# Kernel optimization log

Measured on AMD Instinct MI355X. Metric: run time of the kernel, lower is better.

Reference implementation:

```python
import jax, jax.numpy as jnp
import numpy as np

N = 100000   # nodes
E = 1600000  # edges
G = 64       # graphs in batch
IN, H, F1, OUT = 3, 64, 256, 10
EPS = 1e-5


def setup_inputs() -> dict:
    key = jax.random.key(0)
    ks = jax.random.split(key, 16)
    d = {}
    d["x"] = jax.random.normal(ks[0], (N, IN), dtype=jnp.float32)
    d["membership"] = jnp.sort(jax.random.randint(ks[1], (N,), 0, G))
    d["edges"] = jax.random.randint(ks[2], (2, E), 0, N)
    def lin(k, fan_in, shape):
        return jax.random.uniform(k, shape, jnp.float32, -1.0, 1.0) / np.sqrt(fan_in)
    # GraphConv1: out = lin_rel(agg) + lin_root(x); lin_root has no bias in PyG
    d["W_rel1"] = lin(ks[3], IN, (IN, H)); d["b_rel1"] = jnp.zeros((H,), jnp.float32)
    d["W_root1"] = lin(ks[4], IN, (IN, H))
    d["W_rel2"] = lin(ks[5], H, (H, H)); d["b_rel2"] = jnp.zeros((H,), jnp.float32)
    d["W_root2"] = lin(ks[6], H, (H, H))
    d["g1"] = jnp.ones((H,), jnp.float32); d["b1"] = jnp.zeros((H,), jnp.float32)
    d["g2"] = jnp.ones((H,), jnp.float32); d["b2"] = jnp.zeros((H,), jnp.float32)
    d["W_fc1"] = lin(ks[7], H, (H, F1)); d["b_fc1"] = lin(ks[8], H, (F1,))
    d["g3"] = jnp.ones((F1,), jnp.float32); d["b3"] = jnp.zeros((F1,), jnp.float32)
    d["W_fc2"] = lin(ks[9], F1, (F1, OUT)); d["b_fc2"] = lin(ks[10], F1, (OUT,))
    return d


def _bn(h, g, b):
    # BatchNorm1d in training mode: biased batch variance
    m = h.mean(axis=0)
    v = h.var(axis=0)
    return (h - m) * jax.lax.rsqrt(v + EPS) * g + b


def reference(x, membership, edges, W_rel1, b_rel1, W_root1, W_rel2, b_rel2,
              W_root2, g1, b1, g2, b2, W_fc1, b_fc1, g3, b3, W_fc2, b_fc2):
    src, dst = edges[0], edges[1]

    def gconv(h, Wr, br, Wroot):
        # message = x_j (edge_weight=None); aggr='add' at target node
        agg = jax.ops.segment_sum(h[src], dst, num_segments=N)
        return agg @ Wr + br + h @ Wroot

    h = _bn(jax.nn.relu(gconv(x, W_rel1, b_rel1, W_root1)), g1, b1)
    h = _bn(jax.nn.relu(gconv(h, W_rel2, b_rel2, W_root2)), g2, b2)
    # global mean pool over graph membership
    cnt = jax.ops.segment_sum(jnp.ones((N,), h.dtype), membership, num_segments=G)
    pooled = jax.ops.segment_sum(h, membership, num_segments=G) / jnp.maximum(cnt, 1.0)[:, None]
    z = _bn(jax.nn.relu(pooled @ W_fc1 + b_fc1), g3, b3)
    return z @ W_fc2 + b_fc2
```

## Files before the change

### kernel.cpp

```cpp
#include <hip/hip_runtime.h>
#include <hip/hip_bf16.h>

#define EPSV 1e-5f
#define BKT 128
#define NB  782

typedef __hip_bfloat16 bf16;
typedef __attribute__((ext_vector_type(8))) short short8v;
typedef __attribute__((ext_vector_type(4))) float f32x4v;

__device__ inline void atomAddG(float* p, float v) { unsafeAtomicAdd(p, v); }
__device__ inline unsigned short f2bf(float v) {
    bf16 h = __float2bfloat16(v);
    return *reinterpret_cast<unsigned short*>(&h);
}

__global__ __launch_bounds__(256) void bhist_kernel(
    const int* __restrict__ edges, int* __restrict__ gbcnt, int E)
{
    __shared__ int lh[NB];
    const int t = threadIdx.x;
    for (int i = t; i < NB; i += 256) lh[i] = 0;
    __syncthreads();
    const int base = blockIdx.x * 4096;
    #pragma unroll
    for (int i = 0; i < 16; ++i) {
        int e = base + i * 256 + t;
        if (e < E) atomicAdd(&lh[edges[E + e] >> 7], 1);
    }
    __syncthreads();
    for (int i = t; i < NB; i += 256) {
        int c = lh[i];
        if (c) atomicAdd(&gbcnt[i], c);
    }
}

__global__ __launch_bounds__(256) void bscan_kernel(
    const int* __restrict__ gbcnt, int* __restrict__ bbase,
    int* __restrict__ gcursor, int E)
{
    __shared__ int l[256];
    const int t = threadIdx.x;
    int b0 = t * 4;
    int v0 = (b0 + 0 < NB) ? gbcnt[b0 + 0] : 0;
    int v1 = (b0 + 1 < NB) ? gbcnt[b0 + 1] : 0;
    int v2 = (b0 + 2 < NB) ? gbcnt[b0 + 2] : 0;
    int v3 = (b0 + 3 < NB) ? gbcnt[b0 + 3] : 0;
    int tot = v0 + v1 + v2 + v3;
    l[t] = tot;
    __syncthreads();
    for (int o = 1; o < 256; o <<= 1) {
        int add = (t >= o) ? l[t - o] : 0;
        __syncthreads();
        l[t] += add;
        __syncthreads();
    }
    int off = l[t] - tot;
    if (b0 + 0 < NB) { bbase[b0 + 0] = off;                gcursor[b0 + 0] = off; }
    if (b0 + 1 < NB) { bbase[b0 + 1] = off + v0;           gcursor[b0 + 1] = off + v0; }
    if (b0 + 2 < NB) { bbase[b0 + 2] = off + v0 + v1;      gcursor[b0 + 2] = off + v0 + v1; }
    if (b0 + 3 < NB) { bbase[b0 + 3] = off + v0 + v1 + v2; gcursor[b0 + 3] = off + v0 + v1 + v2; }
    if (t == 0) bbase[NB] = E;
}

__global__ __launch_bounds__(256) void bfill_kernel(
    const int* __restrict__ edges, int* __restrict__ gcursor,
    int* __restrict__ pk, int E)
{
    __shared__ int lh[NB];
    __shared__ int lbase[NB];
    const int t = threadIdx.x;
    for (int i = t; i < NB; i += 256) lh[i] = 0;
    __syncthreads();
    const int base = blockIdx.x * 4096;
    int dv[16];
    #pragma unroll
    for (int i = 0; i < 16; ++i) {
        int e = base + i * 256 + t;
        dv[i] = (e < E) ? edges[E + e] : -1;
        if (dv[i] >= 0) atomicAdd(&lh[dv[i] >> 7], 1);
    }
    __syncthreads();
    for (int i = t; i < NB; i += 256) {
        int c = lh[i];
        lbase[i] = c ? atomicAdd(&gcursor[i], c) : 0;
        lh[i] = 0;
    }
    __syncthreads();
    #pragma unroll
    for (int i = 0; i < 16; ++i) {
        int e = base + i * 256 + t;
        if (dv[i] >= 0) {
            int s = edges[e];
            int b = dv[i] >> 7;
            int pos = lbase[b] + atomicAdd(&lh[b], 1);
            pk[pos] = (s << 7) | (dv[i] & 127);
        }
    }
}

__global__ __launch_bounds__(256) void bsort_kernel(
    const int* __restrict__ pk, const int* __restrict__ bbase,
    const float* __restrict__ x,
    int* __restrict__ rowstart, int* __restrict__ srcs,
    float* __restrict__ agg1, int N, int E)
{
    __shared__ int lcnt[BKT];
    __shared__ int lscan[BKT];
    __shared__ float accx[BKT * 4];
    const int t = threadIdx.x;
    const int b = blockIdx.x;
    const int e0 = bbase[b], e1 = bbase[b + 1];
    if (t < BKT) lcnt[t] = 0;
    for (int i = t; i < BKT * 4; i += 256) accx[i] = 0.f;
    __syncthreads();
    for (int e = e0 + t; e < e1; e += 256) atomicAdd(&lcnt[pk[e] & 127], 1);
    __syncthreads();
    if (t < BKT) lscan[t] = lcnt[t];
    __syncthreads();
    for (int o = 1; o < BKT; o <<= 1) {
        int add = (t < BKT && t >= o) ? lscan[t - o] : 0;
        __syncthreads();
        if (t < BKT) lscan[t] += add;
        __syncthreads();
    }
    const int n0 = b * BKT;
    if (t < BKT) {
        int excl = lscan[t] - lcnt[t];
        lscan[t] = excl;
        int n = n0 + t;
        if (n <= N) rowstart[n] = e0 + excl;
        lcnt[t] = 0;
    }
    __syncthreads();
    for (int e = e0 + t; e < e1; e += 256) {
        int v = pk[e];
        int ld = v & 127;
        int s = v >> 7;
        int pos = atomicAdd(&lcnt[ld], 1);
        srcs[e0 + lscan[ld] + pos] = s;
        atomicAdd(&accx[ld * 4 + 0], x[s * 3 + 0]);
        atomicAdd(&accx[ld * 4 + 1], x[s * 3 + 1]);
        atomicAdd(&accx[ld * 4 + 2], x[s * 3 + 2]);
    }
    __syncthreads();
    for (int i = t; i < BKT * 3; i += 256) {
        int nl = i / 3, c = i - nl * 3;
        int n = n0 + nl;
        if (n < N) agg1[n * 3 + c] = accx[nl * 4 + c];
    }
}

__global__ __launch_bounds__(256) void bounds_kernel(
    const int* __restrict__ membership, int* __restrict__ gstart, int N)
{
    int n = blockIdx.x * 256 + threadIdx.x;
    if (n > N) return;
    int mp = (n == 0) ? -1 : membership[n - 1];
    int mc = (n == N) ? 64 : membership[n];
    for (int g = mp + 1; g <= mc; ++g) gstart[g] = n;
}

__global__ __launch_bounds__(256) void layer1_kernel(
    const float* __restrict__ x, const float* __restrict__ agg1,
    const float* __restrict__ W_rel1, const float* __restrict__ b_rel1,
    const float* __restrict__ W_root1,
    unsigned short* __restrict__ u1b, float* __restrict__ sums, float* __restrict__ sumsq,
    int N)
{
    const int t = threadIdx.x;
    const int f = t & 63, r4 = t >> 6;
    const float wr0 = W_rel1[f], wr1 = W_rel1[64 + f], wr2 = W_rel1[128 + f];
    const float wo0 = W_root1[f], wo1 = W_root1[64 + f], wo2 = W_root1[128 + f];
    const float bb = b_rel1[f];
    float ps = 0.f, pq = 0.f;
    const int base = blockIdx.x * 128;
    for (int i = r4; i < 128; i += 4) {
        int n = base + i;
        if (n >= N) break;
        float a0 = agg1[n * 3 + 0], a1 = agg1[n * 3 + 1], a2 = agg1[n * 3 + 2];
        float x0 = x[n * 3 + 0], x1 = x[n * 3 + 1], x2 = x[n * 3 + 2];
        float v = bb;
        v = fmaf(a0, wr0, v); v = fmaf(a1, wr1, v); v = fmaf(a2, wr2, v);
        v = fmaf(x0, wo0, v); v = fmaf(x1, wo1, v); v = fmaf(x2, wo2, v);
        v = fmaxf(v, 0.f);
        u1b[n * 64 + f] = f2bf(v);
        ps += v; pq += v * v;
    }
    __shared__ float lsum[4][64], lsq[4][64];
    lsum[r4][f] = ps; lsq[r4][f] = pq;
    __syncthreads();
    if (r4 == 0) {
        float s = lsum[0][f] + lsum[1][f] + lsum[2][f] + lsum[3][f];
        float q = lsq[0][f] + lsq[1][f] + lsq[2][f] + lsq[3][f];
        atomAddG(&sums[f], s);
        atomAddG(&sumsq[f], q);
    }
}

__global__ void bnscale_kernel(const float* __restrict__ sums, const float* __restrict__ sumsq,
                               const float* __restrict__ g, const float* __restrict__ b,
                               float invn, int C,
                               float* __restrict__ scale, float* __restrict__ shift)
{
    int f = blockIdx.x * blockDim.x + threadIdx.x;
    if (f >= C) return;
    float m = sums[f] * invn;
    float v = sumsq[f] * invn - m * m;
    float sc = g[f] * rsqrtf(v + EPSV);
    scale[f] = sc;
    shift[f] = b[f] - m * sc;
}

__global__ __launch_bounds__(256) void bnfold_kernel(
    const float* __restrict__ scale1, const float* __restrict__ shift1,
    const float* __restrict__ W_rel2, const float* __restrict__ W_root2,
    const float* __restrict__ b_rel2,
    unsigned short* __restrict__ wrelp, unsigned short* __restrict__ wrootp,
    float* __restrict__ crel, float* __restrict__ croot)
{
    __shared__ float r1[4][64], r2[4][64];
    const int t = threadIdx.x, f = t & 63, kg = t >> 6;
    float c1 = 0.f, c2 = 0.f;
    for (int k = kg * 16; k < kg * 16 + 16; ++k) {
        float sc = scale1[k], sh = shift1[k];
        float w1 = W_rel2[k * 64 + f], w2 = W_root2[k * 64 + f];
        wrelp[k * 64 + f] = f2bf(sc * w1);
        wrootp[k * 64 + f] = f2bf(sc * w2);
        c1 = fmaf(sh, w1, c1); c2 = fmaf(sh, w2, c2);
    }
    r1[kg][f] = c1; r2[kg][f] = c2;
    __syncthreads();
    if (kg == 0) {
        crel[f]  = r1[0][f] + r1[1][f] + r1[2][f] + r1[3][f];
        croot[f] = r2[0][f] + r2[1][f] + r2[2][f] + r2[3][f] + b_rel2[f];
    }
}

__global__ __launch_bounds__(256) void mfma_transform_kernel(
    const unsigned short* __restrict__ u1b,
    const unsigned short* __restrict__ wrelp, const unsigned short* __restrict__ wrootp,
    const float* __restrict__ crel, const float* __restrict__ croot,
    unsigned short* __restrict__ tb, unsigned short* __restrict__ pb, int NT)
{
    const int wid = (blockIdx.x * blockDim.x + threadIdx.x) >> 6;
    const int lane = threadIdx.x & 63;
    const int q = lane >> 4, r = lane & 15;

    short8v Bf[2][8];
    float cadd[8];
    #pragma unroll
    for (int kc = 0; kc < 2; ++kc) {
        #pragma unroll
        for (int ft = 0; ft < 8; ++ft) {
            const unsigned short* W = (ft < 4) ? wrelp : wrootp;
            const int f0 = (ft & 3) * 16;
            short8v b;
            #pragma unroll
            for (int j = 0; j < 8; ++j) {
                int k = 32 * kc + 8 * q + j;
                b[j] = (short)W[k * 64 + f0 + r];
            }
            Bf[kc][ft] = b;
        }
    }
    #pragma unroll
    for (int ft = 0; ft < 8; ++ft)
        cadd[ft] = (ft < 4) ? crel[(ft & 3) * 16 + r] : croot[(ft & 3) * 16 + r];

    const int totalWaves = (gridDim.x * blockDim.x) >> 6;
    for (int tile = wid; tile < NT; tile += totalWaves) {
        const int n0 = tile * 16;
        short8v A0 = *(const short8v*)&u1b[(n0 + r) * 64 + 8 * q];
        short8v A1 = *(const short8v*)&u1b[(n0 + r) * 64 + 32 + 8 * q];
        #pragma unroll
        for (int ft = 0; ft < 8; ++ft) {
            f32x4v d = {0.f, 0.f, 0.f, 0.f};
            d = __builtin_amdgcn_mfma_f32_16x16x32_bf16(A0, Bf[0][ft], d, 0, 0, 0);
            d = __builtin_amdgcn_mfma_f32_16x16x32_bf16(A1, Bf[1][ft], d, 0, 0, 0);
            unsigned short* O = (ft < 4) ? tb : pb;
            const int f0 = (ft & 3) * 16;
            const float ca = cadd[ft];
            #pragma unroll
            for (int rr = 0; rr < 4; ++rr) {
                int n = n0 + 4 * q + rr;
                O[n * 64 + f0 + r] = f2bf(d[rr] + ca);
            }
        }
    }
}

__global__ __launch_bounds__(256, 8) void gatherpool_kernel(
    const bf16* __restrict__ tb, const bf16* __restrict__ pb,
    const int* __restrict__ rowstart, const int* __restrict__ srcs,
    const int* __restrict__ membership,
    float* __restrict__ pooled, float* __restrict__ sums, float* __restrict__ sumsq,
    int N, int chunk)
{
    __shared__ float red[4][64];
    const int tid = threadIdx.x;
    const int w = tid >> 6, f = tid & 63;
    const int gw = __builtin_amdgcn_readfirstlane(blockIdx.x * 4 + w);
    const int n0 = gw * chunk;
    const int n1 = min(N, n0 + chunk);
    float ps = 0.f, pq = 0.f, pacc = 0.f;
    int curg = (n0 < N) ? membership[n0] : -1;

    for (int n = n0; n < n1; ++n) {
        int s0 = rowstart[n], s1 = rowstart[n + 1];
        float acc = __bfloat162float(pb[n * 64 + f]);
        int j = s0;
        for (; j + 15 < s1; j += 16) {
            float vs[16];
            #pragma unroll
            for (int q = 0; q < 16; ++q)
                vs[q] = __bfloat162float(tb[srcs[j + q] * 64 + f]);
            float sA = ((vs[0] + vs[1]) + (vs[2] + vs[3])) + ((vs[4] + vs[5]) + (vs[6] + vs[7]));
            float sB = ((vs[8] + vs[9]) + (vs[10] + vs[11])) + ((vs[12] + vs[13]) + (vs[14] + vs[15]));
            acc += sA + sB;
        }
        for (; j + 3 < s1; j += 4) {
            float v0 = __bfloat162float(tb[srcs[j + 0] * 64 + f]);
            float v1 = __bfloat162float(tb[srcs[j + 1] * 64 + f]);
            float v2 = __bfloat162float(tb[srcs[j + 2] * 64 + f]);
            float v3 = __bfloat162float(tb[srcs[j + 3] * 64 + f]);
            acc += (v0 + v1) + (v2 + v3);
        }
        for (; j < s1; ++j) acc += __bfloat162float(tb[srcs[j] * 64 + f]);

        acc = fmaxf(acc, 0.f);
        ps += acc; pq += acc * acc;

        int g = membership[n];
        if (g != curg) {
            atomAddG(&pooled[curg * 64 + f], pacc);
            pacc = 0.f;
            curg = g;
        }
        pacc += acc;
    }
    if (curg >= 0) atomAddG(&pooled[curg * 64 + f], pacc);

    red[w][f] = ps;
    __syncthreads();
    if (w == 0) atomAddG(&sums[f], red[0][f] + red[1][f] + red[2][f] + red[3][f]);
    __syncthreads();
    red[w][f] = pq;
    __syncthreads();
    if (w == 0) atomAddG(&sumsq[f], red[0][f] + red[1][f] + red[2][f] + red[3][f]);
}

__global__ __launch_bounds__(1024) void fc1_kernel(
    const float* __restrict__ pooled, const int* __restrict__ gstart,
    const float* __restrict__ scale2, const float* __restrict__ shift2,
    const float* __restrict__ W_fc1, const float* __restrict__ b_fc1,
    const float* __restrict__ g3, const float* __restrict__ b3,
    float* __restrict__ z)
{
    __shared__ float pm[4096];
    __shared__ float reds[4][256], redq[4][256];
    __shared__ float lsc[256], lsh[256];
    const int t = threadIdx.x;
    for (int i = t; i < 4096; i += 1024) {
        int g = i >> 6, f = i & 63;
        float c = fmaxf((float)(gstart[g + 1] - gstart[g]), 1.0f);
        pm[i] = fmaf(pooled[i] / c, scale2[f], shift2[f]);
    }
    __syncthreads();
    const int col = t & 255, grp = t >> 8;
    float acc[16];
    const float bc = b_fc1[col];
    #pragma unroll
    for (int g = 0; g < 16; ++g) acc[g] = bc;
    for (int k = 0; k < 64; ++k) {
        float wv = W_fc1[k * 256 + col];
        #pragma unroll
        for (int g = 0; g < 16; ++g)
            acc[g] = fmaf(pm[(grp * 16 + g) * 64 + k], wv, acc[g]);
    }
    float s = 0.f, q = 0.f;
    #pragma unroll
    for (int g = 0; g < 16; ++g) {
        acc[g] = fmaxf(acc[g], 0.f);
        s += acc[g]; q += acc[g] * acc[g];
    }
    reds[grp][col] = s; redq[grp][col] = q;
    __syncthreads();
    if (grp == 0) {
        float S = reds[0][col] + reds[1][col] + reds[2][col] + reds[3][col];
        float Q = redq[0][col] + redq[1][col] + redq[2][col] + redq[3][col];
        float m = S * (1.0f / 64.0f);
        float v = Q * (1.0f / 64.0f) - m * m;
        float sc = g3[col] * rsqrtf(v + EPSV);
        lsc[col] = sc;
        lsh[col] = b3[col] - m * sc;
    }
    __syncthreads();
    float sc = lsc[col], sh = lsh[col];
    #pragma unroll
    for (int g = 0; g < 16; ++g)
        z[(grp * 16 + g) * 256 + col] = fmaf(acc[g], sc, sh);
}

__global__ __launch_bounds__(640) void fc2_kernel(
    const float* __restrict__ z, const float* __restrict__ W_fc2,
    const float* __restrict__ b_fc2, float* __restrict__ out)
{
    int t = threadIdx.x;
    int g = t / 10, o = t % 10;
    float acc = b_fc2[o];
    for (int c = 0; c < 256; ++c)
        acc = fmaf(z[g * 256 + c], W_fc2[c * 10 + o], acc);
    out[g * 10 + o] = acc;
}

extern "C" void kernel_launch(void* const* d_in, const int* in_sizes, int n_in,
                              void* d_out, int out_size, void* d_ws, size_t ws_size,
                              hipStream_t stream) {
    const int N = 100000, E = 1600000;

    const float* x          = (const float*)d_in[0];
    const int*   membership = (const int*)d_in[1];
    const int*   edges      = (const int*)d_in[2];
    const float* W_rel1     = (const float*)d_in[3];
    const float* b_rel1     = (const float*)d_in[4];
    const float* W_root1    = (const float*)d_in[5];
    const float* W_rel2     = (const float*)d_in[6];
    const float* b_rel2     = (const float*)d_in[7];
    const float* W_root2    = (const float*)d_in[8];
    const float* g1         = (const float*)d_in[9];
    const float* b1         = (const float*)d_in[10];
    const float* g2         = (const float*)d_in[11];
    const float* b2         = (const float*)d_in[12];
    const float* W_fc1      = (const float*)d_in[13];
    const float* b_fc1      = (const float*)d_in[14];
    const float* g3         = (const float*)d_in[15];
    const float* b3         = (const float*)d_in[16];
    const float* W_fc2      = (const float*)d_in[17];
    const float* b_fc2      = (const float*)d_in[18];

    int*   wsi      = (int*)d_ws;
    float* wsf      = (float*)d_ws;
    int*   gbcnt    = wsi + 0;
    float* stats    = wsf + 784;
    float* pooled   = wsf + 1296;
    int*   bbase    = wsi + 5392;
    int*   gcursor  = wsi + 6192;
    int*   gstart   = wsi + 6976;
    int*   rowstart = wsi + 7104;
    int*   pk       = wsi + 107168;
    int*   srcs     = wsi + 1707168;
    float* agg1     = wsf + 3307168;
    unsigned short* u1b = (unsigned short*)(wsf + 3607200);
    unsigned short* tb  = (unsigned short*)(wsf + 6807200);
    unsigned short* pb  = (unsigned short*)(wsf + 10007200);
    unsigned short* wrelp  = (unsigned short*)(wsf + 13207200);
    unsigned short* wrootp = (unsigned short*)(wsf + 13209248);
    float* crel     = wsf + 13211296;
    float* croot    = wsf + 13211360;
    float* z        = wsf + 13211424;

    float* sums1  = stats + 0;
    float* sumsq1 = stats + 64;
    float* sums2  = stats + 128;
    float* sumsq2 = stats + 192;
    float* scale1 = stats + 256;
    float* shift1 = stats + 320;
    float* scale2 = stats + 384;
    float* shift2 = stats + 448;

    hipMemsetAsync(d_ws, 0, (size_t)(784 + 512 + 4096) * 4, stream);

    const int EB = (E + 4095) / 4096;
    bhist_kernel<<<EB, 256, 0, stream>>>(edges, gbcnt, E);
    bscan_kernel<<<1, 256, 0, stream>>>(gbcnt, bbase, gcursor, E);
    bfill_kernel<<<EB, 256, 0, stream>>>(edges, gcursor, pk, E);
    bsort_kernel<<<NB, 256, 0, stream>>>(pk, bbase, x, rowstart, srcs, agg1, N, E);
    bounds_kernel<<<(N + 256) / 256, 256, 0, stream>>>(membership, gstart, N);

    layer1_kernel<<<(N + 127) / 128, 256, 0, stream>>>(
        x, agg1, W_rel1, b_rel1, W_root1, u1b, sums1, sumsq1, N);
    bnscale_kernel<<<1, 64, 0, stream>>>(sums1, sumsq1, g1, b1, 1.0f / N, 64, scale1, shift1);

    bnfold_kernel<<<1, 256, 0, stream>>>(scale1, shift1, W_rel2, W_root2, b_rel2,
                                         wrelp, wrootp, crel, croot);
    mfma_transform_kernel<<<512, 256, 0, stream>>>(
        u1b, wrelp, wrootp, crel, croot, tb, pb, N / 16);

    {
        const int GRID2 = 2048;
        int chunk = (N + GRID2 * 4 - 1) / (GRID2 * 4);
        gatherpool_kernel<<<GRID2, 256, 0, stream>>>(
            (const bf16*)tb, (const bf16*)pb, rowstart, srcs, membership,
            pooled, sums2, sumsq2, N, chunk);
    }
    bnscale_kernel<<<1, 64, 0, stream>>>(sums2, sumsq2, g2, b2, 1.0f / N, 64, scale2, shift2);

    fc1_kernel<<<1, 1024, 0, stream>>>(pooled, gstart, scale2, shift2,
                                       W_fc1, b_fc1, g3, b3, z);
    fc2_kernel<<<1, 640, 0, stream>>>(z, W_fc2, b_fc2, (float*)d_out);
}
```

Baseline: 254.3 us.

## Vectorize edge gather to 4 edges per wave and fuse small kernels

The gather kernel now processes four edges in parallel per wave. Each 16-lane quarter loads 8-byte chunks (4 bf16 features) of a source row, and the partial sums are reduced with cross-lane shuffles. This replaces one 2-byte load per lane per edge and is meant to raise memory-level parallelism and use bytes per request better. Separately, the BN1 scale computation is folded into bnfold and fc2 is merged into fc1, removing two tiny kernel launches. The cost is shuffle reductions per node, and three quarters of the lanes sit idle during the per-node epilogue.

After: 265.0 us. 1.04x slower.

```diff
diff --git a/kernel.cpp b/kernel.cpp
--- a/kernel.cpp
+++ b/kernel.cpp
@@ -213,17 +213,27 @@
 }
 
 __global__ __launch_bounds__(256) void bnfold_kernel(
-    const float* __restrict__ scale1, const float* __restrict__ shift1,
+    const float* __restrict__ sums1, const float* __restrict__ sumsq1,
+    const float* __restrict__ g1, const float* __restrict__ b1,
     const float* __restrict__ W_rel2, const float* __restrict__ W_root2,
     const float* __restrict__ b_rel2,
     unsigned short* __restrict__ wrelp, unsigned short* __restrict__ wrootp,
-    float* __restrict__ crel, float* __restrict__ croot)
-{
+    float* __restrict__ crel, float* __restrict__ croot, float invn)
+{
+    __shared__ float lsc[64], lsh[64];
     __shared__ float r1[4][64], r2[4][64];
     const int t = threadIdx.x, f = t & 63, kg = t >> 6;
+    if (t < 64) {
+        float m = sums1[t] * invn;
+        float v = sumsq1[t] * invn - m * m;
+        float sc = g1[t] * rsqrtf(v + EPSV);
+        lsc[t] = sc;
+        lsh[t] = b1[t] - m * sc;
+    }
+    __syncthreads();
     float c1 = 0.f, c2 = 0.f;
     for (int k = kg * 16; k < kg * 16 + 16; ++k) {
-        float sc = scale1[k], sh = shift1[k];
+        float sc = lsc[k], sh = lsh[k];
         float w1 = W_rel2[k * 64 + f], w2 = W_root2[k * 64 + f];
         wrelp[k * 64 + f] = f2bf(sc * w1);
         wrootp[k * 64 + f] = f2bf(sc * w2);
@@ -255,13 +265,13 @@
         for (int ft = 0; ft < 8; ++ft) {
             const unsigned short* W = (ft < 4) ? wrelp : wrootp;
             const int f0 = (ft & 3) * 16;
-            short8v b;
+            short8v bb;
             #pragma unroll
             for (int j = 0; j < 8; ++j) {
                 int k = 32 * kc + 8 * q + j;
-                b[j] = (short)W[k * 64 + f0 + r];
+                bb[j] = (short)W[k * 64 + f0 + r];
             }
-            Bf[kc][ft] = b;
+            Bf[kc][ft] = bb;
         }
     }
     #pragma unroll
@@ -291,7 +301,7 @@
 }
 
 __global__ __launch_bounds__(256, 8) void gatherpool_kernel(
-    const bf16* __restrict__ tb, const bf16* __restrict__ pb,
+    const unsigned short* __restrict__ tb, const unsigned short* __restrict__ pb,
     const int* __restrict__ rowstart, const int* __restrict__ srcs,
     const int* __restrict__ membership,
     float* __restrict__ pooled, float* __restrict__ sums, float* __restrict__ sumsq,
@@ -299,63 +309,110 @@
 {
     __shared__ float red[4][64];
     const int tid = threadIdx.x;
-    const int w = tid >> 6, f = tid & 63;
-    const int gw = __builtin_amdgcn_readfirstlane(blockIdx.x * 4 + w);
+    const int w = tid >> 6, lane = tid & 63;
+    const int q = lane >> 4;
+    const int r = lane & 15;
+    const int gw = blockIdx.x * 4 + w;
     const int n0 = gw * chunk;
     const int n1 = min(N, n0 + chunk);
-    float ps = 0.f, pq = 0.f, pacc = 0.f;
+    float ps0 = 0.f, ps1 = 0.f, ps2 = 0.f, ps3 = 0.f;
+    float pq0 = 0.f, pq1 = 0.f, pq2 = 0.f, pq3 = 0.f;
+    float pa0 = 0.f, pa1 = 0.f, pa2 = 0.f, pa3 = 0.f;
     int curg = (n0 < N) ? membership[n0] : -1;
 
     for (int n = n0; n < n1; ++n) {
         int s0 = rowstart[n], s1 = rowstart[n + 1];
-        float acc = __bfloat162float(pb[n * 64 + f]);
+        float a0 = 0.f, a1 = 0.f, a2 = 0.f, a3 = 0.f;
         int j = s0;
-        for (; j + 15 < s1; j += 16) {
-            float vs[16];
+        for (; j + 31 < s1; j += 32) {
+            int idx[8];
+            uint2 v[8];
             #pragma unroll
-            for (int q = 0; q < 16; ++q)
-                vs[q] = __bfloat162float(tb[srcs[j + q] * 64 + f]);
-            float sA = ((vs[0] + vs[1]) + (vs[2] + vs[3])) + ((vs[4] + vs[5]) + (vs[6] + vs[7]));
-            float sB = ((vs[8] + vs[9]) + (vs[10] + vs[11])) + ((vs[12] + vs[13]) + (vs[14] + vs[15]));
-            acc += sA + sB;
+            for (int u = 0; u < 8; ++u) idx[u] = srcs[j + u * 4 + q];
+            #pragma unroll
+            for (int u = 0; u < 8; ++u)
+                v[u] = *(const uint2*)&tb[idx[u] * 64 + r * 4];
+            #pragma unroll
+            for (int u = 0; u < 8; ++u) {
+                a0 += __uint_as_float(v[u].x << 16);
+                a1 += __uint_as_float(v[u].x & 0xffff0000u);
+                a2 += __uint_as_float(v[u].y << 16);
+                a3 += __uint_as_float(v[u].y & 0xffff0000u);
+            }
         }
         for (; j + 3 < s1; j += 4) {
-            float v0 = __bfloat162float(tb[srcs[j + 0] * 64 + f]);
-            float v1 = __bfloat162float(tb[srcs[j + 1] * 64 + f]);
-            float v2 = __bfloat162float(tb[srcs[j + 2] * 64 + f]);
-            float v3 = __bfloat162float(tb[srcs[j + 3] * 64 + f]);
-            acc += (v0 + v1) + (v2 + v3);
-        }
-        for (; j < s1; ++j) acc += __bfloat162float(tb[srcs[j] * 64 + f]);
-
-        acc = fmaxf(acc, 0.f);
-        ps += acc; pq += acc * acc;
-
-        int g = membership[n];
-        if (g != curg) {
-            atomAddG(&pooled[curg * 64 + f], pacc);
-            pacc = 0.f;
-            curg = g;
-        }
-        pacc += acc;
-    }
-    if (curg >= 0) atomAddG(&pooled[curg * 64 + f], pacc);
-
-    red[w][f] = ps;
-    __syncthreads();
-    if (w == 0) atomAddG(&sums[f], red[0][f] + red[1][f] + red[2][f] + red[3][f]);
-    __syncthreads();
-    red[w][f] = pq;
-    __syncthreads();
-    if (w == 0) atomAddG(&sumsq[f], red[0][f] + red[1][f] + red[2][f] + red[3][f]);
-}
-
-__global__ __launch_bounds__(1024) void fc1_kernel(
+            int src = srcs[j + q];
+            uint2 vv = *(const uint2*)&tb[src * 64 + r * 4];
+            a0 += __uint_as_float(vv.x << 16);
+            a1 += __uint_as_float(vv.x & 0xffff0000u);
+            a2 += __uint_as_float(vv.y << 16);
+            a3 += __uint_as_float(vv.y & 0xffff0000u);
+        }
+        int rem = s1 - j;
+        if (q < rem) {
+            int src = srcs[j + q];
+            uint2 vv = *(const uint2*)&tb[src * 64 + r * 4];
+            a0 += __uint_as_float(vv.x << 16);
+            a1 += __uint_as_float(vv.x & 0xffff0000u);
+            a2 += __uint_as_float(vv.y << 16);
+            a3 += __uint_as_float(vv.y & 0xffff0000u);
+        }
+        a0 += __shfl_xor(a0, 16); a0 += __shfl_xor(a0, 32);
+        a1 += __shfl_xor(a1, 16); a1 += __shfl_xor(a1, 32);
+        a2 += __shfl_xor(a2, 16); a2 += __shfl_xor(a2, 32);
+        a3 += __shfl_xor(a3, 16); a3 += __shfl_xor(a3, 32);
+
+        if (q == 0) {
+            uint2 pv = *(const uint2*)&pb[n * 64 + r * 4];
+            a0 = fmaxf(a0 + __uint_as_float(pv.x << 16), 0.f);
+            a1 = fmaxf(a1 + __uint_as_float(pv.x & 0xffff0000u), 0.f);
+            a2 = fmaxf(a2 + __uint_as_float(pv.y << 16), 0.f);
+            a3 = fmaxf(a3 + __uint_as_float(pv.y & 0xffff0000u), 0.f);
+            ps0 += a0; pq0 += a0 * a0;
+            ps1 += a1; pq1 += a1 * a1;
+            ps2 += a2; pq2 += a2 * a2;
+            ps3 += a3; pq3 += a3 * a3;
+            int g = membership[n];
+            if (g != curg) {
+                atomAddG(&pooled[curg * 64 + 4 * r + 0], pa0);
+                atomAddG(&pooled[curg * 64 + 4 * r + 1], pa1);
+                atomAddG(&pooled[curg * 64 + 4 * r + 2], pa2);
+                atomAddG(&pooled[curg * 64 + 4 * r + 3], pa3);
+                pa0 = pa1 = pa2 = pa3 = 0.f;
+                curg = g;
+            }
+            pa0 += a0; pa1 += a1; pa2 += a2; pa3 += a3;
+        }
+    }
+    if (q == 0 && curg >= 0) {
+        atomAddG(&pooled[curg * 64 + 4 * r + 0], pa0);
+        atomAddG(&pooled[curg * 64 + 4 * r + 1], pa1);
+        atomAddG(&pooled[curg * 64 + 4 * r + 2], pa2);
+        atomAddG(&pooled[curg * 64 + 4 * r + 3], pa3);
+    }
+
+    if (q == 0) {
+        red[w][4 * r + 0] = ps0; red[w][4 * r + 1] = ps1;
+        red[w][4 * r + 2] = ps2; red[w][4 * r + 3] = ps3;
+    }
+    __syncthreads();
+    if (w == 0) atomAddG(&sums[lane], red[0][lane] + red[1][lane] + red[2][lane] + red[3][lane]);
+    __syncthreads();
+    if (q == 0) {
+        red[w][4 * r + 0] = pq0; red[w][4 * r + 1] = pq1;
+        red[w][4 * r + 2] = pq2; red[w][4 * r + 3] = pq3;
+    }
+    __syncthreads();
+    if (w == 0) atomAddG(&sumsq[lane], red[0][lane] + red[1][lane] + red[2][lane] + red[3][lane]);
+}
+
+__global__ __launch_bounds__(1024) void fc12_kernel(
     const float* __restrict__ pooled, const int* __restrict__ gstart,
     const float* __restrict__ scale2, const float* __restrict__ shift2,
     const float* __restrict__ W_fc1, const float* __restrict__ b_fc1,
     const float* __restrict__ g3, const float* __restrict__ b3,
-    float* __restrict__ z)
+    const float* __restrict__ W_fc2, const float* __restrict__ b_fc2,
+    float* __restrict__ z, float* __restrict__ out)
 {
     __shared__ float pm[4096];
     __shared__ float reds[4][256], redq[4][256];
@@ -400,18 +457,14 @@
     #pragma unroll
     for (int g = 0; g < 16; ++g)
         z[(grp * 16 + g) * 256 + col] = fmaf(acc[g], sc, sh);
-}
-
-__global__ __launch_bounds__(640) void fc2_kernel(
-    const float* __restrict__ z, const float* __restrict__ W_fc2,
-    const float* __restrict__ b_fc2, float* __restrict__ out)
-{
-    int t = threadIdx.x;
-    int g = t / 10, o = t % 10;
-    float acc = b_fc2[o];
-    for (int c = 0; c < 256; ++c)
-        acc = fmaf(z[g * 256 + c], W_fc2[c * 10 + o], acc);
-    out[g * 10 + o] = acc;
+    __syncthreads();
+    if (t < 640) {
+        int g = t / 10, o = t % 10;
+        float a = b_fc2[o];
+        for (int c = 0; c < 256; ++c)
+            a = fmaf(z[g * 256 + c], W_fc2[c * 10 + o], a);
+        out[g * 10 + o] = a;
+    }
 }
 
 extern "C" void kernel_launch(void* const* d_in, const int* in_sizes, int n_in,
@@ -464,8 +517,6 @@
     float* sumsq1 = stats + 64;
     float* sums2  = stats + 128;
     float* sumsq2 = stats + 192;
-    float* scale1 = stats + 256;
-    float* shift1 = stats + 320;
     float* scale2 = stats + 384;
     float* shift2 = stats + 448;
 
@@ -480,10 +531,10 @@
 
     layer1_kernel<<<(N + 127) / 128, 256, 0, stream>>>(
         x, agg1, W_rel1, b_rel1, W_root1, u1b, sums1, sumsq1, N);
-    bnscale_kernel<<<1, 64, 0, stream>>>(sums1, sumsq1, g1, b1, 1.0f / N, 64, scale1, shift1);
-
-    bnfold_kernel<<<1, 256, 0, stream>>>(scale1, shift1, W_rel2, W_root2, b_rel2,
-                                         wrelp, wrootp, crel, croot);
+
+    bnfold_kernel<<<1, 256, 0, stream>>>(sums1, sumsq1, g1, b1,
+                                         W_rel2, W_root2, b_rel2,
+                                         wrelp, wrootp, crel, croot, 1.0f / N);
     mfma_transform_kernel<<<512, 256, 0, stream>>>(
         u1b, wrelp, wrootp, crel, croot, tb, pb, N / 16);
 
@@ -491,12 +542,11 @@
         const int GRID2 = 2048;
         int chunk = (N + GRID2 * 4 - 1) / (GRID2 * 4);
         gatherpool_kernel<<<GRID2, 256, 0, stream>>>(
-            (const bf16*)tb, (const bf16*)pb, rowstart, srcs, membership,
-            pooled, sums2, sumsq2, N, chunk);
+            tb, pb, rowstart, srcs, membership, pooled, sums2, sumsq2, N, chunk);
     }
     bnscale_kernel<<<1, 64, 0, stream>>>(sums2, sumsq2, g2, b2, 1.0f / N, 64, scale2, shift2);
 
-    fc1_kernel<<<1, 1024, 0, stream>>>(pooled, gstart, scale2, shift2,
-                                       W_fc1, b_fc1, g3, b3, z);
-    fc2_kernel<<<1, 640, 0, stream>>>(z, W_fc2, b_fc2, (float*)d_out);
-}
+    fc12_kernel<<<1, 1024, 0, stream>>>(pooled, gstart, scale2, shift2,
+                                        W_fc1, b_fc1, g3, b3, W_fc2, b_fc2,
+                                        z, (float*)d_out);
+}
```
